# Performance work log

Hardware: AMD Instinct MI355X
Metric: run time of the kernel (lower is better)

## Reference

```python
import jax, jax.numpy as jnp
import numpy as np

# ---- module config (init_kwargs) ----
B, CIN, H, W_ = 2, 64, 56, 56
COUT, KH, KW = 128, 3, 3
K = CIN * KH * KW               # 576, reduction dim
ARRAY_ROWS = 128
IN_SLICES = (2, 2, 2, 2)        # 8-bit inputs, 2-bit slices
W_SLICES = (2, 2, 2, 2)         # 8-bit weights, 2-bit slices
N_STEPS_IN = 2 ** sum(IN_SLICES)    # 256, unsigned quantizer
N_STEPS_W = 2 ** sum(W_SLICES)      # 256
ADC_BINS = 256
ADC_STEP = 4.0

def _shifts_masks(slices):
    masks, shifts = [], [0]
    for s in slices[::-1]:
        masks.append((1 << s) - 1)
        shifts.append(s + shifts[-1])
    return np.array(shifts[-2::-1], np.int32), np.array(masks[::-1], np.int32)

_ish, _im = _shifts_masks(IN_SLICES)
_wsh, _wm = _shifts_masks(W_SLICES)
ISH, IM = jnp.asarray(_ish), jnp.asarray(_im)
WSH, WM = jnp.asarray(_wsh), jnp.asarray(_wm)
ISF = jnp.asarray((1 << _ish).astype(np.float32))  # slice recombine weights 2^shift
WSF = jnp.asarray((1 << _wsh).astype(np.float32))


def setup_inputs() -> dict:
    key = jax.random.key(0)
    k1, k2 = jax.random.split(key)
    return {
        "x": jax.random.normal(k1, (B, CIN, H, W_), jnp.float32),
        "w": jax.random.normal(k2, (COUT, CIN, KH, KW), jnp.float32),
    }


def _im2col(x):
    # 3x3 SAME conv patches, ordering [Cin, kh, kw] to match w.reshape(COUT, K)
    xp = jnp.pad(x, ((0, 0), (0, 0), (1, 1), (1, 1)))
    cols = jnp.stack([xp[:, :, i:i + H, j:j + W_]
                      for i in range(KH) for j in range(KW)], axis=2)  # [B,Cin,9,H,W]
    return cols.transpose(0, 3, 4, 1, 2).reshape(B * H * W_, K)  # [Nx, K]


def _quant_unsigned(v, n_steps):
    # Quantizer.offset + Quantizer.forward (unsigned, per-row over dim=-1)
    offs = v.min(axis=-1, keepdims=True)
    vr = v - offs
    step = vr.max(axis=-1, keepdims=True) / (n_steps - 1)
    q = jnp.round(jnp.clip(vr, 0.0, step * n_steps) / step).astype(jnp.int32)
    return q, step[..., 0], offs[..., 0]


def _slice_bits(q, shifts, masks):
    # Slicer.forward: stack (q >> shift) & mask along new leading slice dim
    s = shifts.reshape((-1,) + (1,) * q.ndim)
    m = masks.reshape((-1,) + (1,) * q.ndim)
    return (q[None] >> s) & m


def _chunk(t):
    # Chunker.forward over last dim K
    nb = -(-K // ARRAY_ROWS)
    npb = -(-K // nb)
    pad = nb * npb - K
    t = jnp.pad(t, [(0, 0)] * (t.ndim - 1) + [(0, pad)])
    t = t.reshape(t.shape[:-1] + (nb, npb))
    return jnp.moveaxis(t, -2, 0)  # [nb, ..., npb]


def reference(x, w):
    xf = _im2col(x)                    # [Nx, K]
    wf = w.reshape(COUT, K)            # [Ny, K]
    x_sum = xf.sum(axis=-1)            # [Nx]
    w_sum = wf.sum(axis=-1)            # [Ny]

    xq, x_scale, x_offs = _quant_unsigned(xf, N_STEPS_IN)
    wq, w_scale, w_offs = _quant_unsigned(wf, N_STEPS_W)

    xc = _chunk(_slice_bits(xq, ISH, IM))  # [nb, nis, Nx, npb] int32
    wc = _chunk(_slice_bits(wq, WSH, WM))  # [nb, nws, Ny, npb] int32

    # bit-serial crossbar MACs per (chunk, weight-slice, input-slice)
    z = jnp.einsum('bixk,bwyk->bwixy',
                   xc.astype(jnp.float32), wc.astype(jnp.float32))  # [nb,nws,nis,Nx,Ny]

    # ADC digitization (unsigned, fixed step): quantize then dequantize
    z = jnp.round(jnp.clip(z, 0.0, ADC_STEP * ADC_BINS) / ADC_STEP) * ADC_STEP

    # Chunker.reverse: sum crossbar blocks; Slicer.reverse: shift-weighted sums
    z = z.sum(axis=0)                               # [nws,nis,Nx,Ny]
    z = jnp.einsum('wixy,w,i->xy', z, WSF, ISF)     # [Nx,Ny]

    # dequantize scales and unsigned-offset correction:
    # x.y = sx*sy*(xq.yq) + x_offs*sum(y) + y_offs*sum(x) - x_offs*y_offs*K
    z = z * x_scale[:, None] * w_scale[None, :]
    z = (z + x_offs[:, None] * w_sum[None, :]
           + w_offs[None, :] * x_sum[:, None]
           - x_offs[:, None] * w_offs[None, :] * K)

    return z.reshape(B, H, W_, COUT).transpose(0, 3, 1, 2)  # [B,Cout,H,W]
```

## Files before the change

kernel.cpp:

```cpp
#include <hip/hip_runtime.h>


#define KDIM  576
#define NPB   116
#define SSTR  688

typedef int i32x4 __attribute__((ext_vector_type(4)));
typedef float f32x4 __attribute__((ext_vector_type(4)));

__device__ __forceinline__ i32x4 slice2b(i32x4 v, int sh) {
    i32x4 r;
    r[0] = (int)(((unsigned)v[0] >> sh) & 0x03030303u);
    r[1] = (int)(((unsigned)v[1] >> sh) & 0x03030303u);
    r[2] = (int)(((unsigned)v[2] >> sh) & 0x03030303u);
    r[3] = (int)(((unsigned)v[3] >> sh) & 0x03030303u);
    return r;
}

__device__ __forceinline__ void quant36(const float (&v)[36], unsigned char* rowp,
                                        int i16, float* sc, float* of,
                                        float* sm_, int sidx)
{
    float mn = v[0], mx = v[0], sm = 0.f;
#pragma unroll
    for (int m = 0; m < 36; m++) { mn = fminf(mn, v[m]); mx = fmaxf(mx, v[m]); sm += v[m]; }
#pragma unroll
    for (int off = 1; off < 16; off <<= 1) {
        mn = fminf(mn, __shfl_xor(mn, off));
        mx = fmaxf(mx, __shfl_xor(mx, off));
        sm += __shfl_xor(sm, off);
    }
    float step = (mx - mn) / 255.0f;
    if (i16 == 0) { sc[sidx] = step; of[sidx] = mn; sm_[sidx] = sm; }
    int k0 = i16 * 36;
#pragma unroll
    for (int d = 0; d < 9; d++) {
        unsigned int dw = 0;
#pragma unroll
        for (int mb = 0; mb < 4; mb++) {
            int q = (int)rintf((v[d * 4 + mb] - mn) / step);
            q = q < 0 ? 0 : (q > 255 ? 255 : q);
            dw |= (unsigned)q << (8 * mb);
        }
        int kd = k0 + d * 4;
        int ch = kd / NPB;
        *(unsigned int*)(rowp + kd + 12 * ch) = dw;
    }
}

__device__ __forceinline__ void zero_pad_row(unsigned char* scr, int idx) {
    int rl = idx >> 4, dwp = idx & 15;
    int col = dwp < 12 ? (dwp / 3) * 128 + 116 + (dwp % 3) * 4
                       : 624 + (dwp - 12) * 4;
    *(unsigned int*)(scr + rl * SSTR + col) = 0u;
}

__device__ __forceinline__ void copy_out(const unsigned char* scr,
                                         unsigned char* dst, int tid) {
    for (int idx = tid; idx < 640; idx += 256) {
        int u = idx >> 4, rl = idx & 15;
        int dst16 = (u >> 3) * 128 + ((u >> 2) & 1) * 64 + (u & 3) * 16 + rl;
        *(i32x4*)(dst + dst16 * 16) = *(const i32x4*)(scr + rl * SSTR + u * 16);
    }
}

__global__ __launch_bounds__(256) void k_q(
    const float* __restrict__ x, const float* __restrict__ w,
    unsigned char* __restrict__ Xq, unsigned char* __restrict__ Wq,
    float* __restrict__ xscg, float* __restrict__ xofg, float* __restrict__ xsmg,
    float* __restrict__ wscg, float* __restrict__ wofg, float* __restrict__ wsmg)
{
    __shared__ __align__(16) unsigned char scr[16 * SSTR];

    int tid = threadIdx.x, wv = tid >> 6, lane = tid & 63;
    int g = lane >> 4, i16 = lane & 15;
    int blk = blockIdx.x;

    zero_pad_row(scr, tid);

    if (blk < 392) {
        int b = blk >= 196 ? 1 : 0;
        int pos0 = (blk - 196 * b) * 16;
        const float* xb = x + (size_t)(b * 64) * 3136;

        int i = wv * 4 + g;
        int pos = pos0 + i;
        int hg = pos / 56, wg = pos - hg * 56;

        float v[36];
#pragma unroll
        for (int j = 0; j < 4; j++) {
            const float* cb = xb + (size_t)(i16 * 4 + j) * 3136;
#pragma unroll
            for (int kh = 0; kh < 3; kh++) {
                int r = hg - 1 + kh;
                bool rok = (r >= 0 && r < 56);
#pragma unroll
                for (int kw = 0; kw < 3; kw++) {
                    int c = wg - 1 + kw;
                    bool ok = rok && c >= 0 && c < 56;
                    v[j * 9 + kh * 3 + kw] = ok ? cb[r * 56 + c] : 0.f;
                }
            }
        }
        quant36(v, scr + i * SSTR, i16, xscg, xofg, xsmg, blk * 16 + i);
        __syncthreads();

        copy_out(scr, Xq + (size_t)blk * 10240, tid);
    } else {
        int ctile = blk - 392;
        int rl = wv * 4 + g;
        int row = ctile * 16 + rl;
        const float* wr = w + (size_t)row * KDIM + i16 * 36;
        float v[36];
#pragma unroll
        for (int d = 0; d < 9; d++) {
            f32x4 t = *(const f32x4*)(wr + d * 4);
            v[d*4+0] = t[0]; v[d*4+1] = t[1]; v[d*4+2] = t[2]; v[d*4+3] = t[3];
        }
        quant36(v, scr + rl * SSTR, i16, wscg, wofg, wsmg, row);
        __syncthreads();

        copy_out(scr, Wq + (size_t)ctile * 10240, tid);
    }
}

__global__ __launch_bounds__(256) void k_d(
    const unsigned char* __restrict__ Xq, const unsigned char* __restrict__ Wq,
    const float* __restrict__ xscg, const float* __restrict__ xofg,
    const float* __restrict__ xsmg,
    const float* __restrict__ wscg, const float* __restrict__ wofg,
    const float* __restrict__ wsmg, float* __restrict__ out)
{
    __shared__ __align__(16) int pacc[2][64][4];

    int tid = threadIdx.x, wv = tid >> 6, lane = tid & 63;
    int g = lane >> 4, i16 = lane & 15;
    int blk = blockIdx.x;
    int ct = blk & 7, rp = blk >> 3;
    int tl = wv & 1, ihalf = wv >> 1;
    int rtile = rp * 2 + tl;
    const unsigned char* xt = Xq + (size_t)rtile * 10240 + lane * 16;
    const unsigned char* wt = Wq + (size_t)ct * 10240 + lane * 16;

    const i32x4 zero = {0, 0, 0, 0};
    i32x4 acc4[4] = {{0,0,0,0},{0,0,0,0},{0,0,0,0},{0,0,0,0}};
    int is0 = ihalf * 2;
    int ishA = 6 - 2 * is0;
    int ishB = ishA - 2;

#pragma unroll
    for (int ch = 0; ch < 5; ch++) {
        const unsigned char* xc = xt + ch * 2048;
        const unsigned char* wc = wt + ch * 2048;
        i32x4 x0 = *(const i32x4*)(xc), x1 = *(const i32x4*)(xc + 1024);
        i32x4 w0 = *(const i32x4*)(wc), w1 = *(const i32x4*)(wc + 1024);
        i32x4 ws0[4], ws1[4];
#pragma unroll
        for (int ws = 0; ws < 4; ws++) {
            ws0[ws] = slice2b(w0, 6 - 2 * ws);
            ws1[ws] = slice2b(w1, 6 - 2 * ws);
        }
#pragma unroll
        for (int ii = 0; ii < 2; ii++) {
            int ish = ii ? ishB : ishA;
            i32x4 a0 = slice2b(x0, ish), a1 = slice2b(x1, ish);
#pragma unroll
            for (int ws = 0; ws < 4; ws++) {
                i32x4 d = __builtin_amdgcn_mfma_i32_16x16x64_i8(ws0[ws], a0, zero, 0, 0, 0);
                d = __builtin_amdgcn_mfma_i32_16x16x64_i8(ws1[ws], a1, d, 0, 0, 0);
                int sh = ish + 6 - 2 * ws;
#pragma unroll
                for (int r = 0; r < 4; r++) {
                    int z = d[r];
                    z = z > 1024 ? 1024 : z;
                    int t = (z >> 2) & 1;
                    int r4 = (z + 1 + t) & ~3;
                    acc4[ws][r] += r4 << sh;
                }
            }
        }
    }

    i32x4 acc;
#pragma unroll
    for (int r = 0; r < 4; r++)
        acc[r] = (acc4[0][r] + acc4[1][r]) + (acc4[2][r] + acc4[3][r]);

    if (ihalf == 0) *(i32x4*)&pacc[tl][lane][0] = acc;
    __syncthreads();

    if (ihalf == 1) {
        i32x4 p = *(const i32x4*)&pacc[tl][lane][0];
#pragma unroll
        for (int r = 0; r < 4; r++) acc[r] += p[r];

        int b = rtile >= 196 ? 1 : 0;
        int xrow = rtile * 16 + i16;
        float xs_ = xscg[xrow], xo = xofg[xrow], xsv = xsmg[xrow];
        int hw = (rtile - 196 * b) * 16 + i16;
#pragma unroll
        for (int r = 0; r < 4; r++) {
            int wrow = ct * 16 + g * 4 + r;
            float tt = ((float)acc[r] * xs_) * wscg[wrow];
            float res = ((tt + xo * wsmg[wrow]) + wofg[wrow] * xsv)
                      - (xo * wofg[wrow]) * 576.0f;
            out[(size_t)(b * 128 + wrow) * 3136 + hw] = res;
        }
    }
}

extern "C" void kernel_launch(void* const* d_in, const int* in_sizes, int n_in,
                              void* d_out, int out_size, void* d_ws, size_t ws_size,
                              hipStream_t stream) {
    const float* x = (const float*)d_in[0];
    const float* w = (const float*)d_in[1];
    float* out = (float*)d_out;

    unsigned char* Xq = (unsigned char*)d_ws;
    unsigned char* Wq = Xq + (size_t)392 * 10240;
    float* xsc = (float*)(Wq + 8 * 10240);
    float* xof = xsc + 6272;
    float* xsm = xof + 6272;
    float* wsc = xsm + 6272;
    float* wof = wsc + 128;
    float* wsm = wof + 128;

    hipLaunchKernelGGL(k_q, dim3(400), dim3(256), 0, stream,
                       x, w, Xq, Wq, xsc, xof, xsm, wsc, wof, wsm);
    hipLaunchKernelGGL(k_d, dim3(1568), dim3(256), 0, stream,
                       Xq, Wq, xsc, xof, xsm, wsc, wof, wsm, out);
}
```

Baseline: 38.89 us.

## Fuse quantization and bit-sliced MFMA GEMM into one kernel via LDS

Merges the quantize kernel and the dot-product kernel into a single 512-thread kernel. Each block quantizes its 16 im2col rows plus half of the weight rows (64) into shared memory and runs the MFMA slices directly from LDS. The work split changes from input slices to K-chunks. This removes the global round trip of the quantized data, the scale buffers and one launch. The cost is that every block recomputes quantization of 64 weight rows (784 blocks in total), which adds redundant global reads and compute.

```diff
diff --git a/kernel.cpp b/kernel.cpp
--- a/kernel.cpp
+++ b/kernel.cpp
@@ -55,38 +55,48 @@
     *(unsigned int*)(scr + rl * SSTR + col) = 0u;
 }
 
-__device__ __forceinline__ void copy_out(const unsigned char* scr,
-                                         unsigned char* dst, int tid) {
-    for (int idx = tid; idx < 640; idx += 256) {
-        int u = idx >> 4, rl = idx & 15;
-        int dst16 = (u >> 3) * 128 + ((u >> 2) & 1) * 64 + (u & 3) * 16 + rl;
-        *(i32x4*)(dst + dst16 * 16) = *(const i32x4*)(scr + rl * SSTR + u * 16);
-    }
-}
-
-__global__ __launch_bounds__(256) void k_q(
+__global__ __launch_bounds__(512) void k_fused(
     const float* __restrict__ x, const float* __restrict__ w,
-    unsigned char* __restrict__ Xq, unsigned char* __restrict__ Wq,
-    float* __restrict__ xscg, float* __restrict__ xofg, float* __restrict__ xsmg,
-    float* __restrict__ wscg, float* __restrict__ wofg, float* __restrict__ wsmg)
+    float* __restrict__ out)
 {
-    __shared__ __align__(16) unsigned char scr[16 * SSTR];
+    __shared__ __align__(16) unsigned char scrX[16 * SSTR];
+    __shared__ __align__(16) unsigned char scrW[64 * SSTR];
+    __shared__ __align__(16) int pacc[4][64][4];
+    __shared__ float xscl[16], xofl[16], xsml[16];
+    __shared__ float wscl[64], wofl[64], wsml[64];
 
     int tid = threadIdx.x, wv = tid >> 6, lane = tid & 63;
     int g = lane >> 4, i16 = lane & 15;
     int blk = blockIdx.x;
+    int rtile = blk >> 1, chalf = blk & 1;
+    int b = rtile >= 196 ? 1 : 0;
+    int pos0 = (rtile - 196 * b) * 16;
+    const float* xb = x + (size_t)(b * 64) * 3136;
 
-    zero_pad_row(scr, tid);
+    if (tid < 256) zero_pad_row(scrX, tid);
+    for (int j = tid; j < 1024; j += 512) zero_pad_row(scrW, j);
 
-    if (blk < 392) {
-        int b = blk >= 196 ? 1 : 0;
-        int pos0 = (blk - 196 * b) * 16;
-        const float* xb = x + (size_t)(b * 64) * 3136;
+    {
+        int grp = wv * 4 + g;
+#pragma unroll
+        for (int q = 0; q < 2; q++) {
+            int rl = grp * 2 + q;
+            int row = chalf * 64 + rl;
+            const float* wr = w + (size_t)row * KDIM + i16 * 36;
+            float v[36];
+#pragma unroll
+            for (int d = 0; d < 9; d++) {
+                f32x4 t = *(const f32x4*)(wr + d * 4);
+                v[d*4+0] = t[0]; v[d*4+1] = t[1]; v[d*4+2] = t[2]; v[d*4+3] = t[3];
+            }
+            quant36(v, scrW + rl * SSTR, i16, wscl, wofl, wsml, rl);
+        }
+    }
 
+    if (wv < 4) {
         int i = wv * 4 + g;
         int pos = pos0 + i;
         int hg = pos / 56, wg = pos - hg * 56;
-
         float v[36];
 #pragma unroll
         for (int j = 0; j < 4; j++) {
@@ -103,58 +113,23 @@
                 }
             }
         }
-        quant36(v, scr + i * SSTR, i16, xscg, xofg, xsmg, blk * 16 + i);
-        __syncthreads();
+        quant36(v, scrX + i * SSTR, i16, xscl, xofl, xsml, i);
+    }
+    __syncthreads();
 
-        copy_out(scr, Xq + (size_t)blk * 10240, tid);
-    } else {
-        int ctile = blk - 392;
-        int rl = wv * 4 + g;
-        int row = ctile * 16 + rl;
-        const float* wr = w + (size_t)row * KDIM + i16 * 36;
-        float v[36];
-#pragma unroll
-        for (int d = 0; d < 9; d++) {
-            f32x4 t = *(const f32x4*)(wr + d * 4);
-            v[d*4+0] = t[0]; v[d*4+1] = t[1]; v[d*4+2] = t[2]; v[d*4+3] = t[3];
-        }
-        quant36(v, scr + rl * SSTR, i16, wscg, wofg, wsmg, row);
-        __syncthreads();
-
-        copy_out(scr, Wq + (size_t)ctile * 10240, tid);
-    }
-}
-
-__global__ __launch_bounds__(256) void k_d(
-    const unsigned char* __restrict__ Xq, const unsigned char* __restrict__ Wq,
-    const float* __restrict__ xscg, const float* __restrict__ xofg,
-    const float* __restrict__ xsmg,
-    const float* __restrict__ wscg, const float* __restrict__ wofg,
-    const float* __restrict__ wsmg, float* __restrict__ out)
-{
-    __shared__ __align__(16) int pacc[2][64][4];
-
-    int tid = threadIdx.x, wv = tid >> 6, lane = tid & 63;
-    int g = lane >> 4, i16 = lane & 15;
-    int blk = blockIdx.x;
-    int ct = blk & 7, rp = blk >> 3;
-    int tl = wv & 1, ihalf = wv >> 1;
-    int rtile = rp * 2 + tl;
-    const unsigned char* xt = Xq + (size_t)rtile * 10240 + lane * 16;
-    const unsigned char* wt = Wq + (size_t)ct * 10240 + lane * 16;
+    int ctl_l = wv >> 1, khalf = wv & 1;
+    const unsigned char* xp = scrX + i16 * SSTR + g * 16;
+    const unsigned char* wp = scrW + (ctl_l * 16 + i16) * SSTR + g * 16;
 
     const i32x4 zero = {0, 0, 0, 0};
     i32x4 acc4[4] = {{0,0,0,0},{0,0,0,0},{0,0,0,0},{0,0,0,0}};
-    int is0 = ihalf * 2;
-    int ishA = 6 - 2 * is0;
-    int ishB = ishA - 2;
+    int cbeg = khalf ? 3 : 0, cend = khalf ? 5 : 3;
 
-#pragma unroll
-    for (int ch = 0; ch < 5; ch++) {
-        const unsigned char* xc = xt + ch * 2048;
-        const unsigned char* wc = wt + ch * 2048;
-        i32x4 x0 = *(const i32x4*)(xc), x1 = *(const i32x4*)(xc + 1024);
-        i32x4 w0 = *(const i32x4*)(wc), w1 = *(const i32x4*)(wc + 1024);
+    for (int ch = cbeg; ch < cend; ch++) {
+        i32x4 x0 = *(const i32x4*)(xp + ch * 128);
+        i32x4 x1 = *(const i32x4*)(xp + ch * 128 + 64);
+        i32x4 w0 = *(const i32x4*)(wp + ch * 128);
+        i32x4 w1 = *(const i32x4*)(wp + ch * 128 + 64);
         i32x4 ws0[4], ws1[4];
 #pragma unroll
         for (int ws = 0; ws < 4; ws++) {
@@ -162,8 +137,8 @@
             ws1[ws] = slice2b(w1, 6 - 2 * ws);
         }
 #pragma unroll
-        for (int ii = 0; ii < 2; ii++) {
-            int ish = ii ? ishB : ishA;
+        for (int is = 0; is < 4; is++) {
+            int ish = 6 - 2 * is;
             i32x4 a0 = slice2b(x0, ish), a1 = slice2b(x1, ish);
 #pragma unroll
             for (int ws = 0; ws < 4; ws++) {
@@ -187,24 +162,23 @@
     for (int r = 0; r < 4; r++)
         acc[r] = (acc4[0][r] + acc4[1][r]) + (acc4[2][r] + acc4[3][r]);
 
-    if (ihalf == 0) *(i32x4*)&pacc[tl][lane][0] = acc;
+    if (khalf == 0) *(i32x4*)&pacc[ctl_l][lane][0] = acc;
     __syncthreads();
 
-    if (ihalf == 1) {
-        i32x4 p = *(const i32x4*)&pacc[tl][lane][0];
+    if (khalf == 1) {
+        i32x4 p = *(const i32x4*)&pacc[ctl_l][lane][0];
 #pragma unroll
         for (int r = 0; r < 4; r++) acc[r] += p[r];
 
-        int b = rtile >= 196 ? 1 : 0;
-        int xrow = rtile * 16 + i16;
-        float xs_ = xscg[xrow], xo = xofg[xrow], xsv = xsmg[xrow];
-        int hw = (rtile - 196 * b) * 16 + i16;
+        float xs_ = xscl[i16], xo = xofl[i16], xsv = xsml[i16];
+        int hw = pos0 + i16;
 #pragma unroll
         for (int r = 0; r < 4; r++) {
-            int wrow = ct * 16 + g * 4 + r;
-            float tt = ((float)acc[r] * xs_) * wscg[wrow];
-            float res = ((tt + xo * wsmg[wrow]) + wofg[wrow] * xsv)
-                      - (xo * wofg[wrow]) * 576.0f;
+            int rl = ctl_l * 16 + g * 4 + r;
+            int wrow = chalf * 64 + rl;
+            float tt = ((float)acc[r] * xs_) * wscl[rl];
+            float res = ((tt + xo * wsml[rl]) + wofl[rl] * xsv)
+                      - (xo * wofl[rl]) * 576.0f;
             out[(size_t)(b * 128 + wrow) * 3136 + hw] = res;
         }
     }
@@ -217,17 +191,5 @@
     const float* w = (const float*)d_in[1];
     float* out = (float*)d_out;
 
-    unsigned char* Xq = (unsigned char*)d_ws;
-    unsigned char* Wq = Xq + (size_t)392 * 10240;
-    float* xsc = (float*)(Wq + 8 * 10240);
-    float* xof = xsc + 6272;
-    float* xsm = xof + 6272;
-    float* wsc = xsm + 6272;
-    float* wof = wsc + 128;
-    float* wsm = wof + 128;
-
-    hipLaunchKernelGGL(k_q, dim3(400), dim3(256), 0, stream,
-                       x, w, Xq, Wq, xsc, xof, xsm, wsc, wof, wsm);
-    hipLaunchKernelGGL(k_d, dim3(1568), dim3(256), 0, stream,
-                       Xq, Wq, xsc, xof, xsm, wsc, wof, wsm, out);
+    hipLaunchKernelGGL(k_fused, dim3(784), dim3(512), 0, stream, x, w, out);
 }
```

Measured after the change: 55.79 us. +43.5%, slower.

## Store quantized rows unpacked and split dot kernel work across K chunks

Applied to the files above, without the earlier changes.

The quantize kernel now gives one wavefront to each row and writes plain 640-byte rows with byte stores, dropping the LDS scratch staging and the swizzled MFMA-fragment layout. The dot kernel loads fragments directly from those rows at unaligned chunk offsets and splits work by K chunks (3 vs 2) between wave halves instead of by input-slice halves. This removes LDS and sync from quantization at the cost of byte-granular global stores, unaligned dword gathers in the MFMA kernel, and an uneven split between the two wave halves.

```diff
diff --git a/kernel.cpp b/kernel.cpp
--- a/kernel.cpp
+++ b/kernel.cpp
@@ -1,12 +1,10 @@
 #include <hip/hip_runtime.h>
 
 
-#define KDIM  576
-#define NPB   116
-#define SSTR  688
+#define NXROW 6272
+#define RMS   640
 
 typedef int i32x4 __attribute__((ext_vector_type(4)));
-typedef float f32x4 __attribute__((ext_vector_type(4)));
 
 __device__ __forceinline__ i32x4 slice2b(i32x4 v, int sh) {
     i32x4 r;
@@ -17,111 +15,110 @@
     return r;
 }
 
-__device__ __forceinline__ void quant36(const float (&v)[36], unsigned char* rowp,
-                                        int i16, float* sc, float* of,
-                                        float* sm_, int sidx)
-{
-    float mn = v[0], mx = v[0], sm = 0.f;
-#pragma unroll
-    for (int m = 0; m < 36; m++) { mn = fminf(mn, v[m]); mx = fmaxf(mx, v[m]); sm += v[m]; }
-#pragma unroll
-    for (int off = 1; off < 16; off <<= 1) {
-        mn = fminf(mn, __shfl_xor(mn, off));
-        mx = fmaxf(mx, __shfl_xor(mx, off));
-        sm += __shfl_xor(sm, off);
-    }
-    float step = (mx - mn) / 255.0f;
-    if (i16 == 0) { sc[sidx] = step; of[sidx] = mn; sm_[sidx] = sm; }
-    int k0 = i16 * 36;
-#pragma unroll
-    for (int d = 0; d < 9; d++) {
-        unsigned int dw = 0;
-#pragma unroll
-        for (int mb = 0; mb < 4; mb++) {
-            int q = (int)rintf((v[d * 4 + mb] - mn) / step);
-            q = q < 0 ? 0 : (q > 255 ? 255 : q);
-            dw |= (unsigned)q << (8 * mb);
-        }
-        int kd = k0 + d * 4;
-        int ch = kd / NPB;
-        *(unsigned int*)(rowp + kd + 12 * ch) = dw;
-    }
-}
-
-__device__ __forceinline__ void zero_pad_row(unsigned char* scr, int idx) {
-    int rl = idx >> 4, dwp = idx & 15;
-    int col = dwp < 12 ? (dwp / 3) * 128 + 116 + (dwp % 3) * 4
-                       : 624 + (dwp - 12) * 4;
-    *(unsigned int*)(scr + rl * SSTR + col) = 0u;
-}
-
-__device__ __forceinline__ void copy_out(const unsigned char* scr,
-                                         unsigned char* dst, int tid) {
-    for (int idx = tid; idx < 640; idx += 256) {
-        int u = idx >> 4, rl = idx & 15;
-        int dst16 = (u >> 3) * 128 + ((u >> 2) & 1) * 64 + (u & 3) * 16 + rl;
-        *(i32x4*)(dst + dst16 * 16) = *(const i32x4*)(scr + rl * SSTR + u * 16);
-    }
-}
-
 __global__ __launch_bounds__(256) void k_q(
     const float* __restrict__ x, const float* __restrict__ w,
     unsigned char* __restrict__ Xq, unsigned char* __restrict__ Wq,
-    float* __restrict__ xscg, float* __restrict__ xofg, float* __restrict__ xsmg,
-    float* __restrict__ wscg, float* __restrict__ wofg, float* __restrict__ wsmg)
+    float* __restrict__ xsc, float* __restrict__ xof, float* __restrict__ xsm,
+    float* __restrict__ wsc, float* __restrict__ wof, float* __restrict__ wsm)
 {
-    __shared__ __align__(16) unsigned char scr[16 * SSTR];
-
     int tid = threadIdx.x, wv = tid >> 6, lane = tid & 63;
-    int g = lane >> 4, i16 = lane & 15;
-    int blk = blockIdx.x;
-
-    zero_pad_row(scr, tid);
-
-    if (blk < 392) {
-        int b = blk >= 196 ? 1 : 0;
-        int pos0 = (blk - 196 * b) * 16;
+    int W = blockIdx.x * 4 + wv;
+
+    float v[9];
+    unsigned char* rowp;
+    float *sc, *of, *sm;
+    int sidx;
+
+    if (W < NXROW) {
+        int b = W >= 3136 ? 1 : 0;
+        int pos = W - b * 3136;
+        int hg = pos / 56, wg = pos - hg * 56;
         const float* xb = x + (size_t)(b * 64) * 3136;
-
-        int i = wv * 4 + g;
-        int pos = pos0 + i;
-        int hg = pos / 56, wg = pos - hg * 56;
-
-        float v[36];
-#pragma unroll
-        for (int j = 0; j < 4; j++) {
-            const float* cb = xb + (size_t)(i16 * 4 + j) * 3136;
-#pragma unroll
-            for (int kh = 0; kh < 3; kh++) {
-                int r = hg - 1 + kh;
-                bool rok = (r >= 0 && r < 56);
-#pragma unroll
-                for (int kw = 0; kw < 3; kw++) {
-                    int c = wg - 1 + kw;
-                    bool ok = rok && c >= 0 && c < 56;
-                    v[j * 9 + kh * 3 + kw] = ok ? cb[r * 56 + c] : 0.f;
-                }
+#pragma unroll
+        for (int r = 0; r < 9; r++) {
+            int k = r * 64 + lane;
+            int cin = k / 9;
+            int off = k - cin * 9;
+            int kh = off / 3;
+            int kw = off - kh * 3;
+            int hr = hg - 1 + kh, wc = wg - 1 + kw;
+            bool ok = ((unsigned)hr < 56u) && ((unsigned)wc < 56u);
+            v[r] = ok ? xb[cin * 3136 + hr * 56 + wc] : 0.f;
+        }
+        rowp = Xq + (size_t)W * RMS;
+        sc = xsc; of = xof; sm = xsm; sidx = W;
+    } else {
+        int row = W - NXROW;
+        const float* wr = w + (size_t)row * 576;
+#pragma unroll
+        for (int r = 0; r < 9; r++) v[r] = wr[r * 64 + lane];
+        rowp = Wq + (size_t)row * RMS;
+        sc = wsc; of = wof; sm = wsm; sidx = row;
+    }
+
+    float mn = v[0], mx = v[0], s = 0.f;
+#pragma unroll
+    for (int r = 0; r < 9; r++) { mn = fminf(mn, v[r]); mx = fmaxf(mx, v[r]); s += v[r]; }
+#pragma unroll
+    for (int off = 1; off < 64; off <<= 1) {
+        mn = fminf(mn, __shfl_xor(mn, off));
+        mx = fmaxf(mx, __shfl_xor(mx, off));
+        s += __shfl_xor(s, off);
+    }
+    float step = (mx - mn) / 255.0f;
+    if (lane == 0) { sc[sidx] = step; of[sidx] = mn; sm[sidx] = s; }
+
+#pragma unroll
+    for (int r = 0; r < 9; r++) {
+        int q = (int)rintf((v[r] - mn) / step);
+        q = q < 0 ? 0 : (q > 255 ? 255 : q);
+        rowp[r * 64 + lane] = (unsigned char)q;
+    }
+    rowp[576 + lane] = 0;
+}
+
+__device__ __forceinline__ i32x4 ldfrag0(const unsigned char* rp, int ch, int g) {
+    const int* p = (const int*)(rp + ch * 116 + g * 16);
+    i32x4 r = {p[0], p[1], p[2], p[3]};
+    return r;
+}
+__device__ __forceinline__ i32x4 ldfrag1(const unsigned char* rp, int ch, int g) {
+    const int* p = (const int*)(rp + ch * 116 + 64 + g * 16);
+    bool gm = (g == 3);
+    i32x4 r = {p[0], gm ? 0 : p[1], gm ? 0 : p[2], gm ? 0 : p[3]};
+    return r;
+}
+
+__device__ __forceinline__ void chunk_ws(const unsigned char* xr, const unsigned char* wr,
+                                         int ch, int g, i32x4 (&acc4)[4])
+{
+    const i32x4 zero = {0, 0, 0, 0};
+    i32x4 x0 = ldfrag0(xr, ch, g), x1 = ldfrag1(xr, ch, g);
+    i32x4 w0 = ldfrag0(wr, ch, g), w1 = ldfrag1(wr, ch, g);
+    i32x4 ws0[4], ws1[4];
+#pragma unroll
+    for (int ws = 0; ws < 4; ws++) {
+        ws0[ws] = slice2b(w0, 6 - 2 * ws);
+        ws1[ws] = slice2b(w1, 6 - 2 * ws);
+    }
+#pragma unroll
+    for (int is = 0; is < 4; is++) {
+        int ish = 6 - 2 * is;
+        i32x4 a0 = slice2b(x0, ish), a1 = slice2b(x1, ish);
+#pragma unroll
+        for (int ws = 0; ws < 4; ws++) {
+            i32x4 d = __builtin_amdgcn_mfma_i32_16x16x64_i8(ws0[ws], a0, zero, 0, 0, 0);
+            d = __builtin_amdgcn_mfma_i32_16x16x64_i8(ws1[ws], a1, d, 0, 0, 0);
+            int sh = ish + 6 - 2 * ws;
+#pragma unroll
+            for (int r = 0; r < 4; r++) {
+                int z = d[r];
+                z = z > 1024 ? 1024 : z;
+                int t = (z >> 2) & 1;
+                int r4 = (z + 1 + t) & ~3;
+                acc4[ws][r] += r4 << sh;
             }
         }
-        quant36(v, scr + i * SSTR, i16, xscg, xofg, xsmg, blk * 16 + i);
-        __syncthreads();
-
-        copy_out(scr, Xq + (size_t)blk * 10240, tid);
-    } else {
-        int ctile = blk - 392;
-        int rl = wv * 4 + g;
-        int row = ctile * 16 + rl;
-        const float* wr = w + (size_t)row * KDIM + i16 * 36;
-        float v[36];
-#pragma unroll
-        for (int d = 0; d < 9; d++) {
-            f32x4 t = *(const f32x4*)(wr + d * 4);
-            v[d*4+0] = t[0]; v[d*4+1] = t[1]; v[d*4+2] = t[2]; v[d*4+3] = t[3];
-        }
-        quant36(v, scr + rl * SSTR, i16, wscg, wofg, wsmg, row);
-        __syncthreads();
-
-        copy_out(scr, Wq + (size_t)ctile * 10240, tid);
     }
 }
 
@@ -138,59 +135,29 @@
     int g = lane >> 4, i16 = lane & 15;
     int blk = blockIdx.x;
     int ct = blk & 7, rp = blk >> 3;
-    int tl = wv & 1, ihalf = wv >> 1;
+    int tl = wv & 1, khalf = wv >> 1;
     int rtile = rp * 2 + tl;
-    const unsigned char* xt = Xq + (size_t)rtile * 10240 + lane * 16;
-    const unsigned char* wt = Wq + (size_t)ct * 10240 + lane * 16;
-
-    const i32x4 zero = {0, 0, 0, 0};
+    const unsigned char* xr = Xq + (size_t)(rtile * 16 + i16) * RMS;
+    const unsigned char* wr = Wq + (size_t)(ct * 16 + i16) * RMS;
+
     i32x4 acc4[4] = {{0,0,0,0},{0,0,0,0},{0,0,0,0},{0,0,0,0}};
-    int is0 = ihalf * 2;
-    int ishA = 6 - 2 * is0;
-    int ishB = ishA - 2;
-
-#pragma unroll
-    for (int ch = 0; ch < 5; ch++) {
-        const unsigned char* xc = xt + ch * 2048;
-        const unsigned char* wc = wt + ch * 2048;
-        i32x4 x0 = *(const i32x4*)(xc), x1 = *(const i32x4*)(xc + 1024);
-        i32x4 w0 = *(const i32x4*)(wc), w1 = *(const i32x4*)(wc + 1024);
-        i32x4 ws0[4], ws1[4];
-#pragma unroll
-        for (int ws = 0; ws < 4; ws++) {
-            ws0[ws] = slice2b(w0, 6 - 2 * ws);
-            ws1[ws] = slice2b(w1, 6 - 2 * ws);
-        }
-#pragma unroll
-        for (int ii = 0; ii < 2; ii++) {
-            int ish = ii ? ishB : ishA;
-            i32x4 a0 = slice2b(x0, ish), a1 = slice2b(x1, ish);
-#pragma unroll
-            for (int ws = 0; ws < 4; ws++) {
-                i32x4 d = __builtin_amdgcn_mfma_i32_16x16x64_i8(ws0[ws], a0, zero, 0, 0, 0);
-                d = __builtin_amdgcn_mfma_i32_16x16x64_i8(ws1[ws], a1, d, 0, 0, 0);
-                int sh = ish + 6 - 2 * ws;
-#pragma unroll
-                for (int r = 0; r < 4; r++) {
-                    int z = d[r];
-                    z = z > 1024 ? 1024 : z;
-                    int t = (z >> 2) & 1;
-                    int r4 = (z + 1 + t) & ~3;
-                    acc4[ws][r] += r4 << sh;
-                }
-            }
-        }
-    }
-
+    if (khalf == 0) {
+        chunk_ws(xr, wr, 0, g, acc4);
+        chunk_ws(xr, wr, 1, g, acc4);
+        chunk_ws(xr, wr, 2, g, acc4);
+    } else {
+        chunk_ws(xr, wr, 3, g, acc4);
+        chunk_ws(xr, wr, 4, g, acc4);
+    }
     i32x4 acc;
 #pragma unroll
     for (int r = 0; r < 4; r++)
         acc[r] = (acc4[0][r] + acc4[1][r]) + (acc4[2][r] + acc4[3][r]);
 
-    if (ihalf == 0) *(i32x4*)&pacc[tl][lane][0] = acc;
+    if (khalf == 0) *(i32x4*)&pacc[tl][lane][0] = acc;
     __syncthreads();
 
-    if (ihalf == 1) {
+    if (khalf == 1) {
         i32x4 p = *(const i32x4*)&pacc[tl][lane][0];
 #pragma unroll
         for (int r = 0; r < 4; r++) acc[r] += p[r];
@@ -218,15 +185,15 @@
     float* out = (float*)d_out;
 
     unsigned char* Xq = (unsigned char*)d_ws;
-    unsigned char* Wq = Xq + (size_t)392 * 10240;
-    float* xsc = (float*)(Wq + 8 * 10240);
-    float* xof = xsc + 6272;
-    float* xsm = xof + 6272;
-    float* wsc = xsm + 6272;
+    unsigned char* Wq = Xq + (size_t)NXROW * RMS;
+    float* xsc = (float*)(Wq + 128 * RMS);
+    float* xof = xsc + NXROW;
+    float* xsm = xof + NXROW;
+    float* wsc = xsm + NXROW;
     float* wof = wsc + 128;
     float* wsm = wof + 128;
 
-    hipLaunchKernelGGL(k_q, dim3(400), dim3(256), 0, stream,
+    hipLaunchKernelGGL(k_q, dim3(1600), dim3(256), 0, stream,
                        x, w, Xq, Wq, xsc, xof, xsm, wsc, wof, wsm);
     hipLaunchKernelGGL(k_d, dim3(1568), dim3(256), 0, stream,
                        Xq, Wq, xsc, xof, xsm, wsc, wof, wsm, out);
```

Measured after the change: 58.88 us. 51.4% more time.
